# Performance work log

Hardware: AMD Instinct MI355X
Metric: run time of the kernel (lower is better)

## Reference

```python
import jax, jax.numpy as jnp
import numpy as np

D_MODEL = 1024
N_HEADS = 16
HEAD_DIM = D_MODEL // N_HEADS


def setup_inputs() -> dict:
    key = jax.random.key(0)
    k1, k2, k3 = jax.random.split(key, 3)
    B, S = 4, 2048
    x = jax.random.normal(k1, (B, S, D_MODEL), dtype=jnp.float32)
    # scaled init so logits stay reasonable
    w_qkv = jax.random.normal(k2, (D_MODEL, 3 * D_MODEL), dtype=jnp.float32) / np.sqrt(D_MODEL)
    b_qkv = jnp.zeros((3 * D_MODEL,), dtype=jnp.float32)
    w_out = jax.random.normal(k3, (D_MODEL, D_MODEL), dtype=jnp.float32) / np.sqrt(D_MODEL)
    b_out = jnp.zeros((D_MODEL,), dtype=jnp.float32)
    return {"x": x, "w_qkv": w_qkv, "b_qkv": b_qkv, "w_out": w_out, "b_out": b_out}


def reference(x, w_qkv, b_qkv, w_out, b_out):
    B, S, D = x.shape
    qkv = x @ w_qkv + b_qkv                      # [B,S,3D]
    q, k, v = jnp.split(qkv, 3, axis=-1)
    def split_heads(t):
        return t.reshape(B, S, N_HEADS, HEAD_DIM).transpose(0, 2, 1, 3)  # [B,H,S,d]
    q, k, v = split_heads(q), split_heads(k), split_heads(v)
    a = jnp.einsum('bhsd,bhtd->bhst', q, k)      # [B,H,S,S]
    # causal mask added BEFORE scaling, as in the original module
    causal_mask = jnp.triu(jnp.full((S, S), -jnp.inf, dtype=a.dtype), k=1)
    a = (a + causal_mask) / np.sqrt(HEAD_DIM)
    a = jax.nn.softmax(a, axis=-1)
    z = jnp.einsum('bhst,bhtd->bhsd', a, v)      # [B,H,S,d]
    z = z.transpose(0, 2, 1, 3).reshape(B, S, D)
    return z @ w_out + b_out
```

## Files before the change

### kernel.cpp

```cpp
#include <hip/hip_runtime.h>
#include <hip/hip_bf16.h>
#include <stdint.h>

#define B_   4
#define S_   2048
#define H_   16
#define HD_  64
#define D_   1024

typedef short  short8  __attribute__((ext_vector_type(8)));
typedef float  f32x4   __attribute__((ext_vector_type(4)));
typedef float  f32x16  __attribute__((ext_vector_type(16)));

__device__ __forceinline__ unsigned short f2bf(float f) {
    union { float f; unsigned u; } v; v.f = f;
    unsigned r = v.u + 0x7fffu + ((v.u >> 16) & 1u);
    return (unsigned short)(r >> 16);
}

#if __has_builtin(__builtin_amdgcn_exp2f)
#define EXP2(x) __builtin_amdgcn_exp2f(x)
#else
#define EXP2(x) exp2f(x)
#endif

__device__ __forceinline__ unsigned cvtpk(float lo, float hi) {
    unsigned r;
    asm("v_cvt_pk_bf16_f32 %0, %1, %2" : "=v"(r) : "v"(lo), "v"(hi));
    return r;
}

__device__ __forceinline__ float bq(float v, int srclane) {
    return __int_as_float(__builtin_amdgcn_ds_bpermute(srclane << 2, __float_as_int(v)));
}

__device__ __forceinline__ void pl32swap(unsigned &x, unsigned &y) {
    asm volatile("v_permlane32_swap_b32 %0, %1" : "+v"(x), "+v"(y));
}

#define MFMA32(a, b, c) __builtin_amdgcn_mfma_f32_32x32x16_bf16(a, b, c, 0, 0, 0)
#define MFMA16(a, b, c) __builtin_amdgcn_mfma_f32_16x16x32_bf16(a, b, c, 0, 0, 0)

__global__ __launch_bounds__(256) void k_cvt(const float* __restrict__ in,
                                             unsigned short* __restrict__ out) {
    int i = (blockIdx.x * 256 + threadIdx.x) * 4;
    float4 f = *(const float4*)(in + i);
    ushort4 o;
    o.x = f2bf(f.x); o.y = f2bf(f.y); o.z = f2bf(f.z); o.w = f2bf(f.w);
    *(ushort4*)(out + i) = o;
}

__global__ __launch_bounds__(256) void k_transpose_cvt(const float* __restrict__ in,
                                                       unsigned short* __restrict__ out,
                                                       int K, int N) {
    __shared__ float tile[32][33];
    int n0 = blockIdx.x * 32, k0 = blockIdx.y * 32;
    int tx = threadIdx.x, ty = threadIdx.y;
#pragma unroll
    for (int i = 0; i < 32; i += 8)
        tile[ty + i][tx] = in[(size_t)(k0 + ty + i) * N + n0 + tx];
    __syncthreads();
#pragma unroll
    for (int i = 0; i < 32; i += 8)
        out[(size_t)(n0 + ty + i) * K + k0 + tx] = f2bf(tile[tx][ty + i]);
}

__device__ __forceinline__ void async_load16(const unsigned short* g, unsigned short* l) {
    __builtin_amdgcn_global_load_lds(
        (const __attribute__((address_space(1))) unsigned int*)g,
        (__attribute__((address_space(3))) unsigned int*)l, 16, 0, 0);
}

template <int TPOSED>
__global__ __launch_bounds__(512, 1) void k_gemm8(const unsigned short* __restrict__ A,
                                                  const unsigned short* __restrict__ BT,
                                                  const float* __restrict__ bias,
                                                  unsigned short* __restrict__ qb,
                                                  unsigned short* __restrict__ kb,
                                                  unsigned short* __restrict__ vtb,
                                                  int M, int N, int K, int nbase) {
    __shared__ __attribute__((aligned(16))) unsigned short A0s[256 * 64];
    __shared__ __attribute__((aligned(16))) unsigned short A1s[256 * 64];
    __shared__ __attribute__((aligned(16))) unsigned short A2s[256 * 64];
    __shared__ __attribute__((aligned(16))) unsigned short W0s[128 * 64];
    __shared__ __attribute__((aligned(16))) unsigned short W1s[128 * 64];
    __shared__ __attribute__((aligned(16))) unsigned short W2s[128 * 64];
    const int tid = threadIdx.x, wave = tid >> 6, lane = tid & 63;
    const int wR = wave >> 2, wC = wave & 3;
    const int m0 = blockIdx.y * 256, n0 = nbase + blockIdx.x * 128;

    const unsigned short* AG = A + (size_t)m0 * K;
    const unsigned short* WG = BT + (size_t)n0 * K;

    const int rbase = wave * 8 + (lane >> 3);
    const int scol8 = ((lane & 7) ^ ((lane >> 3) & 7)) * 8;
    const int sdst  = wave * 512;
    const int q15 = lane & 15, q4 = (lane >> 4) << 2;
    const int cb0 = ((lane >> 4) * 16) ^ ((lane & 7) << 4);
    const int cb1 = (64 + (lane >> 4) * 16) ^ ((lane & 7) << 4);

    f32x4 acc[2][4][2] = {};

#define STAGE3(SA, SW, KT, KH)                                                        \
    if ((KH) == 0) {                                                                  \
        async_load16(AG + (size_t)(rbase)       * K + (KT) + scol8, (SA) + 0 * 4096 + sdst); \
        async_load16(AG + (size_t)(64 + rbase)  * K + (KT) + scol8, (SA) + 1 * 4096 + sdst); \
        async_load16(WG + (size_t)(rbase)       * K + (KT) + scol8, (SW) + 0 * 4096 + sdst); \
    } else {                                                                          \
        async_load16(AG + (size_t)(128 + rbase) * K + (KT) + scol8, (SA) + 2 * 4096 + sdst); \
        async_load16(AG + (size_t)(192 + rbase) * K + (KT) + scol8, (SA) + 3 * 4096 + sdst); \
        async_load16(WG + (size_t)(64 + rbase)  * K + (KT) + scol8, (SW) + 1 * 4096 + sdst); \
    }

#define PHASEBODY(CA, CW, SA, SW, MORE, KT2, KH, CB)                                  \
    {                                                                                 \
        short8 xf[2][4], yf[2][2];                                                    \
        if (TPOSED) {                                                                 \
            _Pragma("unroll")                                                         \
            for (int i = 0; i < 4; ++i)                                               \
                xf[0][i] = *(const short8*)((const char*)(CW) + (wR * 64 + i * 16 + q15) * 128 + (CB)); \
            _Pragma("unroll")                                                         \
            for (int h = 0; h < 2; ++h)                                               \
                _Pragma("unroll")                                                     \
                for (int j = 0; j < 2; ++j)                                           \
                    yf[h][j] = *(const short8*)((const char*)(CA) + (h * 128 + wC * 32 + j * 16 + q15) * 128 + (CB)); \
        } else {                                                                      \
            _Pragma("unroll")                                                         \
            for (int h = 0; h < 2; ++h)                                               \
                _Pragma("unroll")                                                     \
                for (int i = 0; i < 4; ++i)                                           \
                    xf[h][i] = *(const short8*)((const char*)(CA) + (h * 128 + wR * 64 + i * 16 + q15) * 128 + (CB)); \
            _Pragma("unroll")                                                         \
            for (int j = 0; j < 2; ++j)                                               \
                yf[0][j] = *(const short8*)((const char*)(CW) + (wC * 32 + j * 16 + q15) * 128 + (CB)); \
        }                                                                             \
        if (MORE) {                                                                   \
            STAGE3(SA, SW, KT2, KH)                                                   \
            asm volatile("s_waitcnt vmcnt(6)" ::: "memory");                          \
        } else {                                                                      \
            asm volatile("s_waitcnt vmcnt(0)" ::: "memory");                          \
        }                                                                             \
        __builtin_amdgcn_s_barrier();                                                 \
        asm volatile("s_waitcnt lgkmcnt(0)" ::: "memory");                            \
        __builtin_amdgcn_sched_barrier(0);                                            \
        __builtin_amdgcn_s_setprio(1);                                                \
        _Pragma("unroll")                                                             \
        for (int h = 0; h < 2; ++h)                                                   \
            _Pragma("unroll")                                                         \
            for (int i = 0; i < 4; ++i)                                               \
                _Pragma("unroll")                                                     \
                for (int j = 0; j < 2; ++j)                                           \
                    acc[h][i][j] = MFMA16(TPOSED ? xf[0][i] : xf[h][i],               \
                                          TPOSED ? yf[h][j] : yf[0][j],               \
                                          acc[h][i][j]);                              \
        __builtin_amdgcn_s_setprio(0);                                                \
        asm volatile("" ::: "memory");                                                \
        __builtin_amdgcn_s_barrier();                                                 \
    }

#define TILEBODY(CA, CW, SA, SW, TC)                                                  \
    {                                                                                 \
        const int more_ = ((TC) + 2) < 16;                                            \
        const int kt2_ = ((TC) + 2) * 64;                                             \
        PHASEBODY(CA, CW, SA, SW, more_, kt2_, 0, cb0)                                \
        PHASEBODY(CA, CW, SA, SW, more_, kt2_, 1, cb1)                                \
    }

    STAGE3(A0s, W0s, 0, 0)
    STAGE3(A0s, W0s, 0, 1)
    STAGE3(A1s, W1s, 64, 0)
    STAGE3(A1s, W1s, 64, 1)
    asm volatile("s_waitcnt vmcnt(6)" ::: "memory");
    __builtin_amdgcn_s_barrier();

    for (int t = 0; t < 15; t += 3) {
        TILEBODY(A0s, W0s, A2s, W2s, t)
        TILEBODY(A1s, W1s, A0s, W0s, t + 1)
        TILEBODY(A2s, W2s, A1s, W1s, t + 2)
    }
    TILEBODY(A0s, W0s, A2s, W2s, 15)
#undef STAGE3
#undef PHASEBODY
#undef TILEBODY

    if (TPOSED) {
        unsigned short* dst = (n0 < 1024) ? qb : kb;
        const float scale = (n0 < 1024) ? 0.18033688011112042f : 1.0f;
#pragma unroll
        for (int i = 0; i < 4; ++i) {
            int nr = n0 + wR * 64 + i * 16 + q4;
            float4 bv4 = *(const float4*)(bias + nr);
            int d0 = nr & 63, hh = (nr & 1023) >> 6;
#pragma unroll
            for (int h = 0; h < 2; ++h)
#pragma unroll
            for (int j = 0; j < 2; ++j) {
                int mc = m0 + h * 128 + wC * 32 + j * 16 + q15;
                int b = mc >> 11, s = mc & 2047;
                size_t bh = (size_t)(b * 16 + hh);
                f32x4 a = acc[h][i][j];
                ushort4 o;
                o.x = f2bf((a[0] + bv4.x) * scale);
                o.y = f2bf((a[1] + bv4.y) * scale);
                o.z = f2bf((a[2] + bv4.z) * scale);
                o.w = f2bf((a[3] + bv4.w) * scale);
                size_t off = bh * 131072 +
                    (size_t)((s >> 5) * 4 + (d0 >> 4)) * 512 +
                    ((s & 31) * 2 + ((d0 >> 3) & 1)) * 8 + (d0 & 7);
                *(ushort4*)(dst + off) = o;
            }
        }
    } else {
#pragma unroll
        for (int h = 0; h < 2; ++h)
#pragma unroll
        for (int i = 0; i < 4; ++i) {
            int mr = m0 + h * 128 + wR * 64 + i * 16 + q4;
            int b = mr >> 11, s0 = mr & 2047;
#pragma unroll
            for (int j = 0; j < 2; ++j) {
                int nc = n0 + wC * 32 + j * 16 + q15;
                int rem = nc & 1023, hh = rem >> 6, d = rem & 63;
                float bv = bias[nc];
                f32x4 a = acc[h][i][j];
                ushort4 o;
                o.x = f2bf(a[0] + bv);
                o.y = f2bf(a[1] + bv);
                o.z = f2bf(a[2] + bv);
                o.w = f2bf(a[3] + bv);
                size_t bh = (size_t)(b * 16 + hh);
                size_t off = bh * 131072 +
                    (size_t)((s0 >> 5) * 4 + (d >> 5) * 2 + ((s0 >> 4) & 1)) * 512 +
                    (((d & 31) << 1) + ((s0 >> 3) & 1)) * 8 + (s0 & 7);
                *(ushort4*)(vtb + off) = o;
            }
        }
    }
}

__global__ __launch_bounds__(256) void k_gemm_out(const unsigned short* __restrict__ A,
                                                  const unsigned short* __restrict__ BT,
                                                  const float* __restrict__ bias,
                                                  float* __restrict__ outf,
                                                  int M, int N, int K) {
    __shared__ __attribute__((aligned(16))) unsigned short As0[128 * 64];
    __shared__ __attribute__((aligned(16))) unsigned short Bs0[128 * 64];
    __shared__ __attribute__((aligned(16))) unsigned short As1[128 * 64];
    __shared__ __attribute__((aligned(16))) unsigned short Bs1[128 * 64];
    const int tid = threadIdx.x, wave = tid >> 6, lane = tid & 63;
    const int m0 = blockIdx.y * 128, n0 = blockIdx.x * 128;
    const int wr = wave >> 1, wc = wave & 1;

    int srow[4], scol8[4], sbu[4];
#pragma unroll
    for (int p = 0; p < 4; p++) {
        int bu = p * 256 + wave * 64;
        int u0 = bu + lane;
        sbu[p]   = bu * 8;
        srow[p]  = u0 >> 3;
        scol8[p] = ((u0 & 7) ^ (srow[p] & 7)) * 8;
    }

#define STAGE(AD, BD, KT)                                                           \
    _Pragma("unroll")                                                               \
    for (int p = 0; p < 4; p++) {                                                   \
        async_load16(A  + (size_t)(m0 + srow[p]) * K + (KT) + scol8[p], AD + sbu[p]); \
        async_load16(BT + (size_t)(n0 + srow[p]) * K + (KT) + scol8[p], BD + sbu[p]); \
    }

    f32x4 acc[4][4] = {};

#define COMPUTE(AS, BS)                                                              \
    _Pragma("unroll")                                                                \
    for (int kk = 0; kk < 2; kk++) {                                                 \
        short8 af[4], bf[4];                                                         \
        _Pragma("unroll")                                                            \
        for (int i = 0; i < 4; i++) {                                                \
            int ra = wr * 64 + i * 16 + (lane & 15);                                 \
            int rb = wc * 64 + i * 16 + (lane & 15);                                 \
            int cb = (kk * 32 + (lane >> 4) * 8) * 2;                                \
            af[i] = *(const short8*)((const char*)AS + ra * 128 + (cb ^ ((ra & 7) << 4))); \
            bf[i] = *(const short8*)((const char*)BS + rb * 128 + (cb ^ ((rb & 7) << 4))); \
        }                                                                            \
        __builtin_amdgcn_s_setprio(1);                                               \
        _Pragma("unroll")                                                            \
        for (int i = 0; i < 4; i++)                                                  \
            _Pragma("unroll")                                                        \
            for (int j = 0; j < 4; j++)                                              \
                acc[i][j] = MFMA16(af[i], bf[j], acc[i][j]);                         \
        __builtin_amdgcn_s_setprio(0);                                               \
    }

    const int NT = K >> 6;
    STAGE(As0, Bs0, 0)
    __syncthreads();
    for (int t = 0; t < NT; t += 2) {
        if (t + 1 < NT) STAGE(As1, Bs1, (t + 1) * 64)
        COMPUTE(As0, Bs0)
        __syncthreads();
        if (t + 2 < NT) STAGE(As0, Bs0, (t + 2) * 64)
        if (t + 1 < NT) {
            COMPUTE(As1, Bs1)
            __syncthreads();
        }
    }
#undef STAGE
#undef COMPUTE

#pragma unroll
    for (int i = 0; i < 4; i++) {
#pragma unroll
        for (int j = 0; j < 4; j++) {
            int n = n0 + wc * 64 + j * 16 + (lane & 15);
            float bv = bias[n];
#pragma unroll
            for (int r = 0; r < 4; r++) {
                int m = m0 + wr * 64 + i * 16 + ((lane >> 4) << 2) + r;
                outf[(size_t)m * N + n] = acc[i][j][r] + bv;
            }
        }
    }
}

__device__ __forceinline__ void do_strip(int strip, int bh, int c, int hi,
                                         const unsigned short* __restrict__ QFb,
                                         const unsigned short* __restrict__ KFb,
                                         const unsigned short* __restrict__ VFb,
                                         unsigned short* __restrict__ Z) {
    const int qbase = strip * 32;
    const int b = bh >> 4, h = bh & 15;
    const int lp8 = ((c << 1) + hi) << 3;

    short8 qf[4];
#pragma unroll
    for (int kd = 0; kd < 4; kd++)
        qf[kd] = *(const short8*)(QFb + (strip * 4 + kd) * 512 + lp8);

    f32x16 o0a = {}, o0b = {}, o1a = {}, o1b = {};
    float l_r = 0.f;
    const int nkv = strip + 1;

    short8 kf_cur[4], kf_nxt[4];
#pragma unroll
    for (int kd = 0; kd < 4; kd++)
        kf_cur[kd] = *(const short8*)(KFb + kd * 512 + lp8);

    for (int tt = 0; tt < nkv; ++tt) {
        const int tn = (tt + 1 < nkv) ? (tt + 1) : tt;
#pragma unroll
        for (int kd = 0; kd < 4; kd++)
            kf_nxt[kd] = *(const short8*)(KFb + (tn * 4 + kd) * 512 + lp8);

        short8 vf[2][2];
#pragma unroll
        for (int dt = 0; dt < 2; dt++)
#pragma unroll
            for (int ks = 0; ks < 2; ks++)
                vf[dt][ks] = *(const short8*)(VFb + (tt * 4 + dt * 2 + ks) * 512 + lp8);

        f32x16 sTa = {}, sTb = {};
        sTa = MFMA32(kf_cur[0], qf[0], sTa);
        sTb = MFMA32(kf_cur[2], qf[2], sTb);
        sTa = MFMA32(kf_cur[1], qf[1], sTa);
        sTb = MFMA32(kf_cur[3], qf[3], sTb);
        f32x16 sT;
#pragma unroll
        for (int r = 0; r < 16; r++) sT[r] = sTa[r] + sTb[r];

        if (tt * 32 == qbase) {
#pragma unroll
            for (int r = 0; r < 16; r++) {
                int tl = (r & 3) + 8 * (r >> 2) + 4 * hi;
                if (tl > c) sT[r] = -1e30f;
            }
        }

#pragma unroll
        for (int r = 0; r < 16; r++) sT[r] = EXP2(sT[r]);
        float s0 = sT[0] + sT[8],  s1 = sT[1] + sT[9];
        float s2 = sT[2] + sT[10], s3 = sT[3] + sT[11];
        float s4 = sT[4] + sT[12], s5 = sT[5] + sT[13];
        float s6 = sT[6] + sT[14], s7 = sT[7] + sT[15];
        s0 += s4; s1 += s5; s2 += s6; s3 += s7;
        l_r += (s0 + s2) + (s1 + s3);

        unsigned pk0 = cvtpk(sT[0],  sT[1]);
        unsigned pk1 = cvtpk(sT[2],  sT[3]);
        unsigned pk2 = cvtpk(sT[4],  sT[5]);
        unsigned pk3 = cvtpk(sT[6],  sT[7]);
        unsigned pk4 = cvtpk(sT[8],  sT[9]);
        unsigned pk5 = cvtpk(sT[10], sT[11]);
        unsigned pk6 = cvtpk(sT[12], sT[13]);
        unsigned pk7 = cvtpk(sT[14], sT[15]);
        pl32swap(pk0, pk2);
        pl32swap(pk1, pk3);
        pl32swap(pk4, pk6);
        pl32swap(pk5, pk7);
        union { unsigned u[4]; short8 s; } pa0, pa1;
        pa0.u[0] = pk0; pa0.u[1] = pk1; pa0.u[2] = pk2; pa0.u[3] = pk3;
        pa1.u[0] = pk4; pa1.u[1] = pk5; pa1.u[2] = pk6; pa1.u[3] = pk7;

        o0a = MFMA32(pa0.s, vf[0][0], o0a);
        o1a = MFMA32(pa0.s, vf[1][0], o1a);
        o0b = MFMA32(pa1.s, vf[0][1], o0b);
        o1b = MFMA32(pa1.s, vf[1][1], o1b);

#pragma unroll
        for (int kd = 0; kd < 4; kd++) kf_cur[kd] = kf_nxt[kd];
    }

    l_r += __shfl_xor(l_r, 32);
    float inv = __builtin_amdgcn_rcpf(l_r);
#pragma unroll
    for (int r = 0; r < 16; r++) {
        int crow = (r & 3) + 8 * (r >> 2) + 4 * hi;
        float ib = bq(inv, crow);
        int q = qbase + crow;
        unsigned short* zp = Z + ((size_t)b * S_ + q) * D_ + h * HD_;
        zp[c]      = f2bf((o0a[r] + o0b[r]) * ib);
        zp[32 + c] = f2bf((o1a[r] + o1b[r]) * ib);
    }
}

__global__ __launch_bounds__(64, 2) void k_attn(const unsigned short* __restrict__ QF,
                                                const unsigned short* __restrict__ KF,
                                                const unsigned short* __restrict__ VF,
                                                unsigned short* __restrict__ Z) {
    const int i = blockIdx.x;
    const int bh = (i & 7) * 8 + ((i >> 3) & 7);
    const int pr = i >> 6;
    const int lane = threadIdx.x & 63;
    const int c = lane & 31, hi = lane >> 5;
    const unsigned short* QFb = QF + (size_t)bh * 131072;
    const unsigned short* KFb = KF + (size_t)bh * 131072;
    const unsigned short* VFb = VF + (size_t)bh * 131072;
    do_strip(pr,      bh, c, hi, QFb, KFb, VFb, Z);
    do_strip(63 - pr, bh, c, hi, QFb, KFb, VFb, Z);
}

extern "C" void kernel_launch(void* const* d_in, const int* in_sizes, int n_in,
                              void* d_out, int out_size, void* d_ws, size_t ws_size,
                              hipStream_t stream) {
    const float* x     = (const float*)d_in[0];
    const float* w_qkv = (const float*)d_in[1];
    const float* b_qkv = (const float*)d_in[2];
    const float* w_out = (const float*)d_in[3];
    const float* b_out = (const float*)d_in[4];
    float* out = (float*)d_out;

    char* ws = (char*)d_ws;
    unsigned short* xb    = (unsigned short*)(ws + 0);
    unsigned short* wqkvT = (unsigned short*)(ws + 16777216);
    unsigned short* woutT = (unsigned short*)(ws + 23068672);
    unsigned short* qb    = (unsigned short*)(ws + 25165824);
    unsigned short* kb    = (unsigned short*)(ws + 41943040);
    unsigned short* vtb   = (unsigned short*)(ws + 58720256);
    unsigned short* zb    = xb;

    k_cvt<<<8192, 256, 0, stream>>>(x, xb);
    k_transpose_cvt<<<dim3(96, 32), dim3(32, 8), 0, stream>>>(w_qkv, wqkvT, 1024, 3072);
    k_transpose_cvt<<<dim3(32, 32), dim3(32, 8), 0, stream>>>(w_out, woutT, 1024, 1024);
    k_gemm8<1><<<dim3(16, 32), 512, 0, stream>>>(xb, wqkvT, b_qkv, qb, kb, vtb,
                                                 8192, 3072, 1024, 0);
    k_gemm8<0><<<dim3(8, 32), 512, 0, stream>>>(xb, wqkvT, b_qkv, qb, kb, vtb,
                                                8192, 3072, 1024, 2048);
    k_attn<<<2048, 64, 0, stream>>>(qb, kb, vtb, zb);
    k_gemm_out<<<dim3(8, 64), 256, 0, stream>>>(zb, woutT, b_out, out, 8192, 1024, 1024);
}
```

Baseline: 172.8 us.

## Rewrite output GEMM as 8-wave triple-buffered kernel, split attention strips across waves

Replaces the 4-wave 128x128 double-buffered output projection with an 8-wave 256x128 tile. It uses a three-stage LDS ring, half-tile async staging with explicit vmcnt waits and barriers, and float4 bias and stores. It also changes the attention kernel so each block runs two waves, one per paired strip (pr and 63-pr), instead of one wave doing both strips in sequence. This is meant to hide more load latency in the GEMM and to double attention parallelism. The costs are more LDS and register pressure, and the hand-written vmcnt counts must match the issued loads exactly.

```diff
diff --git a/kernel.cpp b/kernel.cpp
--- a/kernel.cpp
+++ b/kernel.cpp
@@ -238,86 +238,118 @@
     }
 }
 
-__global__ __launch_bounds__(256) void k_gemm_out(const unsigned short* __restrict__ A,
-                                                  const unsigned short* __restrict__ BT,
-                                                  const float* __restrict__ bias,
-                                                  float* __restrict__ outf,
-                                                  int M, int N, int K) {
-    __shared__ __attribute__((aligned(16))) unsigned short As0[128 * 64];
-    __shared__ __attribute__((aligned(16))) unsigned short Bs0[128 * 64];
-    __shared__ __attribute__((aligned(16))) unsigned short As1[128 * 64];
-    __shared__ __attribute__((aligned(16))) unsigned short Bs1[128 * 64];
+__global__ __launch_bounds__(512, 1) void k_gemm_out8(const unsigned short* __restrict__ A,
+                                                      const unsigned short* __restrict__ BT,
+                                                      const float* __restrict__ bias,
+                                                      float* __restrict__ outf,
+                                                      int M, int N, int K) {
+    __shared__ __attribute__((aligned(16))) unsigned short A0s[256 * 64];
+    __shared__ __attribute__((aligned(16))) unsigned short A1s[256 * 64];
+    __shared__ __attribute__((aligned(16))) unsigned short A2s[256 * 64];
+    __shared__ __attribute__((aligned(16))) unsigned short W0s[128 * 64];
+    __shared__ __attribute__((aligned(16))) unsigned short W1s[128 * 64];
+    __shared__ __attribute__((aligned(16))) unsigned short W2s[128 * 64];
     const int tid = threadIdx.x, wave = tid >> 6, lane = tid & 63;
-    const int m0 = blockIdx.y * 128, n0 = blockIdx.x * 128;
-    const int wr = wave >> 1, wc = wave & 1;
-
-    int srow[4], scol8[4], sbu[4];
-#pragma unroll
-    for (int p = 0; p < 4; p++) {
-        int bu = p * 256 + wave * 64;
-        int u0 = bu + lane;
-        sbu[p]   = bu * 8;
-        srow[p]  = u0 >> 3;
-        scol8[p] = ((u0 & 7) ^ (srow[p] & 7)) * 8;
-    }
-
-#define STAGE(AD, BD, KT)                                                           \
-    _Pragma("unroll")                                                               \
-    for (int p = 0; p < 4; p++) {                                                   \
-        async_load16(A  + (size_t)(m0 + srow[p]) * K + (KT) + scol8[p], AD + sbu[p]); \
-        async_load16(BT + (size_t)(n0 + srow[p]) * K + (KT) + scol8[p], BD + sbu[p]); \
-    }
-
-    f32x4 acc[4][4] = {};
-
-#define COMPUTE(AS, BS)                                                              \
-    _Pragma("unroll")                                                                \
-    for (int kk = 0; kk < 2; kk++) {                                                 \
-        short8 af[4], bf[4];                                                         \
-        _Pragma("unroll")                                                            \
-        for (int i = 0; i < 4; i++) {                                                \
-            int ra = wr * 64 + i * 16 + (lane & 15);                                 \
-            int rb = wc * 64 + i * 16 + (lane & 15);                                 \
-            int cb = (kk * 32 + (lane >> 4) * 8) * 2;                                \
-            af[i] = *(const short8*)((const char*)AS + ra * 128 + (cb ^ ((ra & 7) << 4))); \
-            bf[i] = *(const short8*)((const char*)BS + rb * 128 + (cb ^ ((rb & 7) << 4))); \
-        }                                                                            \
-        __builtin_amdgcn_s_setprio(1);                                               \
-        _Pragma("unroll")                                                            \
-        for (int i = 0; i < 4; i++)                                                  \
-            _Pragma("unroll")                                                        \
-            for (int j = 0; j < 4; j++)                                              \
-                acc[i][j] = MFMA16(af[i], bf[j], acc[i][j]);                         \
-        __builtin_amdgcn_s_setprio(0);                                               \
-    }
-
-    const int NT = K >> 6;
-    STAGE(As0, Bs0, 0)
-    __syncthreads();
-    for (int t = 0; t < NT; t += 2) {
-        if (t + 1 < NT) STAGE(As1, Bs1, (t + 1) * 64)
-        COMPUTE(As0, Bs0)
-        __syncthreads();
-        if (t + 2 < NT) STAGE(As0, Bs0, (t + 2) * 64)
-        if (t + 1 < NT) {
-            COMPUTE(As1, Bs1)
-            __syncthreads();
-        }
-    }
-#undef STAGE
-#undef COMPUTE
-
-#pragma unroll
-    for (int i = 0; i < 4; i++) {
-#pragma unroll
-        for (int j = 0; j < 4; j++) {
-            int n = n0 + wc * 64 + j * 16 + (lane & 15);
-            float bv = bias[n];
-#pragma unroll
-            for (int r = 0; r < 4; r++) {
-                int m = m0 + wr * 64 + i * 16 + ((lane >> 4) << 2) + r;
-                outf[(size_t)m * N + n] = acc[i][j][r] + bv;
-            }
+    const int wR = wave >> 2, wC = wave & 3;
+    const int m0 = blockIdx.y * 256, n0 = blockIdx.x * 128;
+
+    const unsigned short* AG = A + (size_t)m0 * K;
+    const unsigned short* WG = BT + (size_t)n0 * K;
+
+    const int rbase = wave * 8 + (lane >> 3);
+    const int scol8 = ((lane & 7) ^ ((lane >> 3) & 7)) * 8;
+    const int sdst  = wave * 512;
+    const int q15 = lane & 15, q4 = (lane >> 4) << 2;
+    const int cb0 = ((lane >> 4) * 16) ^ ((lane & 7) << 4);
+    const int cb1 = (64 + (lane >> 4) * 16) ^ ((lane & 7) << 4);
+
+    f32x4 acc[2][4][2] = {};
+
+#define STAGE3O(SA, SW, KT, KH)                                                       \
+    if ((KH) == 0) {                                                                  \
+        async_load16(AG + (size_t)(rbase)       * K + (KT) + scol8, (SA) + 0 * 4096 + sdst); \
+        async_load16(AG + (size_t)(64 + rbase)  * K + (KT) + scol8, (SA) + 1 * 4096 + sdst); \
+        async_load16(WG + (size_t)(rbase)       * K + (KT) + scol8, (SW) + 0 * 4096 + sdst); \
+    } else {                                                                          \
+        async_load16(AG + (size_t)(128 + rbase) * K + (KT) + scol8, (SA) + 2 * 4096 + sdst); \
+        async_load16(AG + (size_t)(192 + rbase) * K + (KT) + scol8, (SA) + 3 * 4096 + sdst); \
+        async_load16(WG + (size_t)(64 + rbase)  * K + (KT) + scol8, (SW) + 1 * 4096 + sdst); \
+    }
+
+#define PHASEBODYO(CA, CW, SA, SW, MORE, KT2, KH, CB)                                 \
+    {                                                                                 \
+        short8 xf[4], yf[2][2];                                                       \
+        _Pragma("unroll")                                                             \
+        for (int i = 0; i < 4; ++i)                                                   \
+            xf[i] = *(const short8*)((const char*)(CW) + (wR * 64 + i * 16 + q15) * 128 + (CB)); \
+        _Pragma("unroll")                                                             \
+        for (int h = 0; h < 2; ++h)                                                   \
+            _Pragma("unroll")                                                         \
+            for (int j = 0; j < 2; ++j)                                               \
+                yf[h][j] = *(const short8*)((const char*)(CA) + (h * 128 + wC * 32 + j * 16 + q15) * 128 + (CB)); \
+        if (MORE) {                                                                   \
+            STAGE3O(SA, SW, KT2, KH)                                                  \
+            asm volatile("s_waitcnt vmcnt(6)" ::: "memory");                          \
+        } else {                                                                      \
+            asm volatile("s_waitcnt vmcnt(0)" ::: "memory");                          \
+        }                                                                             \
+        __builtin_amdgcn_s_barrier();                                                 \
+        asm volatile("s_waitcnt lgkmcnt(0)" ::: "memory");                            \
+        __builtin_amdgcn_sched_barrier(0);                                            \
+        __builtin_amdgcn_s_setprio(1);                                                \
+        _Pragma("unroll")                                                             \
+        for (int h = 0; h < 2; ++h)                                                   \
+            _Pragma("unroll")                                                         \
+            for (int i = 0; i < 4; ++i)                                               \
+                _Pragma("unroll")                                                     \
+                for (int j = 0; j < 2; ++j)                                           \
+                    acc[h][i][j] = MFMA16(xf[i], yf[h][j], acc[h][i][j]);             \
+        __builtin_amdgcn_s_setprio(0);                                                \
+        asm volatile("" ::: "memory");                                                \
+        __builtin_amdgcn_s_barrier();                                                 \
+    }
+
+#define TILEBODYO(CA, CW, SA, SW, TC)                                                 \
+    {                                                                                 \
+        const int more_ = ((TC) + 2) < 16;                                            \
+        const int kt2_ = ((TC) + 2) * 64;                                             \
+        PHASEBODYO(CA, CW, SA, SW, more_, kt2_, 0, cb0)                               \
+        PHASEBODYO(CA, CW, SA, SW, more_, kt2_, 1, cb1)                               \
+    }
+
+    STAGE3O(A0s, W0s, 0, 0)
+    STAGE3O(A0s, W0s, 0, 1)
+    STAGE3O(A1s, W1s, 64, 0)
+    STAGE3O(A1s, W1s, 64, 1)
+    asm volatile("s_waitcnt vmcnt(6)" ::: "memory");
+    __builtin_amdgcn_s_barrier();
+
+    for (int t = 0; t < 15; t += 3) {
+        TILEBODYO(A0s, W0s, A2s, W2s, t)
+        TILEBODYO(A1s, W1s, A0s, W0s, t + 1)
+        TILEBODYO(A2s, W2s, A1s, W1s, t + 2)
+    }
+    TILEBODYO(A0s, W0s, A2s, W2s, 15)
+#undef STAGE3O
+#undef PHASEBODYO
+#undef TILEBODYO
+
+#pragma unroll
+    for (int i = 0; i < 4; ++i) {
+        int nr = n0 + wR * 64 + i * 16 + q4;
+        float4 bv4 = *(const float4*)(bias + nr);
+#pragma unroll
+        for (int h = 0; h < 2; ++h)
+#pragma unroll
+        for (int j = 0; j < 2; ++j) {
+            int mc = m0 + h * 128 + wC * 32 + j * 16 + q15;
+            f32x4 a = acc[h][i][j];
+            float4 o;
+            o.x = a[0] + bv4.x;
+            o.y = a[1] + bv4.y;
+            o.z = a[2] + bv4.z;
+            o.w = a[3] + bv4.w;
+            *(float4*)(outf + (size_t)mc * N + nr) = o;
         }
     }
 }
@@ -422,20 +454,21 @@
     }
 }
 
-__global__ __launch_bounds__(64, 2) void k_attn(const unsigned short* __restrict__ QF,
-                                                const unsigned short* __restrict__ KF,
-                                                const unsigned short* __restrict__ VF,
-                                                unsigned short* __restrict__ Z) {
+__global__ __launch_bounds__(128, 4) void k_attn(const unsigned short* __restrict__ QF,
+                                                 const unsigned short* __restrict__ KF,
+                                                 const unsigned short* __restrict__ VF,
+                                                 unsigned short* __restrict__ Z) {
     const int i = blockIdx.x;
     const int bh = (i & 7) * 8 + ((i >> 3) & 7);
     const int pr = i >> 6;
-    const int lane = threadIdx.x & 63;
+    const int tid = threadIdx.x;
+    const int wave = tid >> 6, lane = tid & 63;
     const int c = lane & 31, hi = lane >> 5;
+    const int strip = wave ? (63 - pr) : pr;
     const unsigned short* QFb = QF + (size_t)bh * 131072;
     const unsigned short* KFb = KF + (size_t)bh * 131072;
     const unsigned short* VFb = VF + (size_t)bh * 131072;
-    do_strip(pr,      bh, c, hi, QFb, KFb, VFb, Z);
-    do_strip(63 - pr, bh, c, hi, QFb, KFb, VFb, Z);
+    do_strip(strip, bh, c, hi, QFb, KFb, VFb, Z);
 }
 
 extern "C" void kernel_launch(void* const* d_in, const int* in_sizes, int n_in,
@@ -464,6 +497,6 @@
                                                  8192, 3072, 1024, 0);
     k_gemm8<0><<<dim3(8, 32), 512, 0, stream>>>(xb, wqkvT, b_qkv, qb, kb, vtb,
                                                 8192, 3072, 1024, 2048);
-    k_attn<<<2048, 64, 0, stream>>>(qb, kb, vtb, zb);
-    k_gemm_out<<<dim3(8, 64), 256, 0, stream>>>(zb, woutT, b_out, out, 8192, 1024, 1024);
-}
+    k_attn<<<2048, 128, 0, stream>>>(qb, kb, vtb, zb);
+    k_gemm_out8<<<dim3(8, 32), 512, 0, stream>>>(zb, woutT, b_out, out, 8192, 1024, 1024);
+}
```

New measurement: 307.8 us. 78.2% more time.
